# Kernel optimization log

Measured on AMD Instinct MI355X. Metric: run time of the kernel, lower is better.

Reference implementation:

```python
import jax, jax.numpy as jnp
import numpy as np

CH = 32          # channels
HID = CH * 16    # GRU hidden/input size = 512


def setup_inputs() -> dict:
    key = jax.random.key(0)
    ks = jax.random.split(key, 9)
    B, T = 512, 128
    s = 1.0 / np.sqrt(HID)
    frames = jax.random.uniform(ks[0], (B, T, 1, 16, 16), dtype=jnp.float32)
    conv_w = jax.random.normal(ks[1], (CH, 2, 4, 4), jnp.float32) * 0.1
    conv_b = jax.random.normal(ks[2], (CH,), jnp.float32) * 0.01
    w_ih = jax.random.uniform(ks[3], (3 * HID, HID), jnp.float32, -s, s)
    w_hh = jax.random.uniform(ks[4], (3 * HID, HID), jnp.float32, -s, s)
    b_ih = jax.random.uniform(ks[5], (3 * HID,), jnp.float32, -s, s)
    b_hh = jax.random.uniform(ks[6], (3 * HID,), jnp.float32, -s, s)
    deconv_w = jax.random.normal(ks[7], (CH, 1, 4, 4), jnp.float32) * 0.1
    deconv_b = jax.random.normal(ks[8], (1,), jnp.float32) * 0.01
    return {"frames": frames, "conv_w": conv_w, "conv_b": conv_b,
            "w_ih": w_ih, "w_hh": w_hh, "b_ih": b_ih, "b_hh": b_hh,
            "deconv_w": deconv_w, "deconv_b": deconv_b}


def reference(frames, conv_w, conv_b, w_ih, w_hh, b_ih, b_hh, deconv_w, deconv_b):
    B, T = frames.shape[0], frames.shape[1]
    T2 = T - 2
    curr = frames[:, 1:T - 1]              # (B,T2,1,16,16)
    prev = frames[:, :T - 2]               # (B,T2,1,16,16)
    diff = jnp.concatenate([curr, prev], axis=2)  # (B,T2,2,16,16)

    # Encoder: Conv2d(2,CH,4,stride=4). Stride==kernel -> non-overlapping patches.
    # Reshape HxW=16x16 into (i,p,j,q) with H=4i+p, W=4j+q.
    x = diff.reshape(B * T2, 2, 4, 4, 4, 4)                 # (n,c,i,p,j,q)
    enc = jnp.einsum('bcipjq,ocpq->boij', x, conv_w) + conv_b[None, :, None, None]
    feat = jax.nn.gelu(enc, approximate=False).reshape(B, T2, HID)  # flatten(1), exact GELU

    # GRU (single layer, batch_first, zero init hidden)
    gates_x = jnp.einsum('bti,gi->tbg', feat, w_ih) + b_ih  # (T2,B,3H)

    def step(h, gx):
        gh = h @ w_hh.T + b_hh
        gxr, gxz, gxn = jnp.split(gx, 3, axis=-1)
        ghr, ghz, ghn = jnp.split(gh, 3, axis=-1)
        r = jax.nn.sigmoid(gxr + ghr)
        z = jax.nn.sigmoid(gxz + ghz)
        n = jnp.tanh(gxn + r * ghn)
        h_new = (1.0 - z) * n + z * h
        return h_new, h_new

    h0 = jnp.zeros((B, HID), frames.dtype)
    _, outs = jax.lax.scan(step, h0, gates_x)               # (T2,B,HID)

    # Decoder: ConvTranspose2d(CH,1,4,stride=4). Stride==kernel -> scatter patches.
    dec_in = outs.transpose(1, 0, 2).reshape(B * T2, CH, 4, 4)
    dec = jnp.einsum('ncij,copq->noipjq', dec_in, deconv_w).reshape(B * T2, 1, 16, 16)
    delta = jnp.tanh(dec + deconv_b[None, :, None, None])

    pred = jnp.clip(curr.reshape(B * T2, 1, 16, 16) + delta, 0.0, 1.0)
    return pred.reshape(B, T2, 1, 16, 16)
```

## Files before the change

### kernel.cpp

```cpp
#include <hip/hip_runtime.h>
#include <cstdint>

typedef float f32x4 __attribute__((ext_vector_type(4)));
typedef __bf16 bf16x8 __attribute__((ext_vector_type(8)));
typedef unsigned short us8 __attribute__((ext_vector_type(8)));
typedef unsigned int u32x4 __attribute__((ext_vector_type(4)));
typedef unsigned long long u64;

#define T2 126

__device__ __forceinline__ unsigned short f2bf(float x){
  union { float f; uint32_t u; } v; v.f = x;
  return (unsigned short)((v.u + 0x7fffu + ((v.u >> 16) & 1u)) >> 16);
}
__device__ __forceinline__ float bf2f(unsigned short h){
  union { uint32_t u; float f; } v; v.u = ((uint32_t)h) << 16; return v.f;
}
__device__ __forceinline__ f32x4 mfma_bf16(us8 a, us8 b, f32x4 c){
  return __builtin_amdgcn_mfma_f32_16x16x32_bf16(
      __builtin_bit_cast(bf16x8, a), __builtin_bit_cast(bf16x8, b), c, 0, 0, 0);
}
__device__ __forceinline__ float sigm(float x){ return 1.0f / (1.0f + __expf(-x)); }

#define HSWZ(row, chunk) ((row) * 512 + ((((chunk) ^ ((row) & 7))) << 3))

__global__ void __launch_bounds__(256) pack_w_kernel(const float* __restrict__ w,
                                                     unsigned short* __restrict__ dst){
  int tid = blockIdx.x * 256 + threadIdx.x;
  int l = tid & 63;
  int tile = tid >> 6;
  int kt = tile & 15, jt = tile >> 4;
  int row = jt * 16 + (l & 15);
  int col = kt * 32 + (l >> 4) * 8;
  const float* s = w + (size_t)row * 512 + col;
  unsigned short o[8];
  #pragma unroll
  for (int e = 0; e < 8; e++) o[e] = f2bf(s[e]);
  *(us8*)(dst + (size_t)tid * 8) = *(const us8*)o;
}

__global__ void __launch_bounds__(512, 1) gates_gemm_kernel(
    const float* __restrict__ frames,
    const float* __restrict__ cw,
    const float* __restrict__ cb,
    const unsigned short* __restrict__ wih_p,
    const float* __restrict__ b_ih,
    unsigned short* __restrict__ gates_c,
    int t0, int Tc){
  __shared__ unsigned short alds[112 * 512];
  __shared__ float wl[1024];
  __shared__ float cbl[32];
  int tid = threadIdx.x;
  int grp = blockIdx.x & 31;
  int tlc = blockIdx.x >> 5;
  wl[tid] = cw[tid]; wl[tid + 512] = cw[tid + 512];
  if (tid < 32) cbl[tid] = cb[tid];
  __syncthreads();
  #pragma unroll
  for (int tk = 0; tk < 4; tk++){
    int task = tid + 512 * tk;
    if (task < 1792){
      int sA = task >> 4, patch = task & 15;
      int t7 = sA >> 4, i = sA & 15;
      int tl = tlc * 7 + t7;
      int b = grp * 16 + i;
      int t = t0 + tl;
      const float* fb = frames + ((size_t)b * 128 + t) * 256;
      int ii = patch >> 2, jj = patch & 3;
      float4 pv[4], cv[4];
      #pragma unroll
      for (int p = 0; p < 4; p++){
        int base = (ii * 4 + p) * 16 + jj * 4;
        pv[p] = *(const float4*)(fb + base);
        cv[p] = *(const float4*)(fb + 256 + base);
      }
      #pragma unroll
      for (int o = 0; o < 32; o++){
        const float* wc = &wl[o * 32];
        float acc = cbl[o];
        #pragma unroll
        for (int p = 0; p < 4; p++){
          acc += cv[p].x * wc[p*4+0] + cv[p].y * wc[p*4+1]
               + cv[p].z * wc[p*4+2] + cv[p].w * wc[p*4+3];
          acc += pv[p].x * wc[16+p*4+0] + pv[p].y * wc[16+p*4+1]
               + pv[p].z * wc[16+p*4+2] + pv[p].w * wc[16+p*4+3];
        }
        float g = 0.5f * acc * (1.0f + erff(acc * 0.70710678118654752f));
        int col = o * 16 + patch;
        alds[HSWZ(sA, col >> 3) + (col & 7)] = f2bf(g);
      }
    }
  }
  __syncthreads();
  int l = tid & 63, w = tid >> 6;
  int lr = l & 15, lh = l >> 4;
  for (int jg = 0; jg < 3; jg++){
    int jt0 = w * 12 + jg * 4;
    int q4 = w * 3 + jg;
    int g = q4 >> 3, slcT = q4 & 7;
    f32x4 acc[7][4];
    #pragma unroll
    for (int mt = 0; mt < 7; mt++)
      #pragma unroll
      for (int jj = 0; jj < 4; jj++) acc[mt][jj] = (f32x4){0.f,0.f,0.f,0.f};
    #pragma unroll
    for (int kt = 0; kt < 16; kt++){
      us8 a[7], bfr[4];
      #pragma unroll
      for (int mt = 0; mt < 7; mt++)
        a[mt] = *(const us8*)&alds[HSWZ(mt * 16 + lr, kt * 4 + lh)];
      #pragma unroll
      for (int jj = 0; jj < 4; jj++)
        bfr[jj] = *(const us8*)(wih_p + ((size_t)((jt0 + jj) * 16 + kt) * 512 + l * 8));
      #pragma unroll
      for (int mt = 0; mt < 7; mt++)
        #pragma unroll
        for (int jj = 0; jj < 4; jj++)
          acc[mt][jj] = mfma_bf16(a[mt], bfr[jj], acc[mt][jj]);
    }
    #pragma unroll
    for (int jj = 0; jj < 4; jj++){
      float bias = b_ih[(jt0 + jj) * 16 + lr];
      #pragma unroll
      for (int mt = 0; mt < 7; mt++){
        size_t base2 = (((size_t)(tlc * 7 + mt) * 32 + grp) * 8 + slcT) * 3072
                     + g * 1024 + jj * 256 + lr;
        #pragma unroll
        for (int rr = 0; rr < 4; rr++)
          gates_c[base2 + (lh * 4 + rr) * 16] = f2bf(acc[mt][jj][rr] + bias);
      }
    }
  }
}

__global__ void __launch_bounds__(256) scan_init_kernel(u32x4* __restrict__ hq,
                                                        unsigned int* __restrict__ tagbuf){
  int tid = blockIdx.x * 256 + threadIdx.x;
  int stride = gridDim.x * 256;
  for (int i = tid; i < 32768; i += stride)
    hq[i] = (u32x4){0u, 0u, 0u, 0u};
  for (int i = tid; i < 2 * 8 * 32 * 16; i += stride)
    tagbuf[i] = 0u;
}

__global__ void __launch_bounds__(256, 1) gru_scan_kernel(
    const unsigned short* __restrict__ gates_c,
    const unsigned short* __restrict__ whh_p,
    const float* __restrict__ b_hh,
    u32x4* __restrict__ hq,
    unsigned int* __restrict__ tagbuf,
    float* __restrict__ h_state,
    const float* __restrict__ frames,
    const float* __restrict__ dw,
    const float* __restrict__ db,
    float* __restrict__ out,
    int Tc, int t0){
  __shared__ unsigned short hlds[16 * 512];
  __shared__ unsigned short hout[16 * 64];
  __shared__ float dwl[512];
  const int tid = threadIdx.x;
  const int B = blockIdx.x;
  const int grp = B & 31;
  const int slc = B >> 5;
  const int l = tid & 63;
  const int w = tid >> 6;
  const int lr = l & 15, lh = l >> 4;
  const int j = slc * 64 + w * 16 + lr;
  const int rowb = grp * 16;
  const int rloc = lh * 4;

  dwl[tid] = dw[tid]; dwl[tid + 256] = dw[tid + 256];
  const float dbias = db[0];

  us8 wr[16], wz[16], wn[16];
  {
    const int jt = slc * 4 + w;
    #pragma unroll
    for (int kt = 0; kt < 16; kt++){
      wr[kt] = *(volatile const us8*)(whh_p + ((size_t)((jt      ) * 16 + kt) * 512 + l * 8));
      wz[kt] = *(volatile const us8*)(whh_p + ((size_t)((jt + 32) * 16 + kt) * 512 + l * 8));
      wn[kt] = *(volatile const us8*)(whh_p + ((size_t)((jt + 64) * 16 + kt) * 512 + l * 8));
    }
  }
  const float bhr = b_hh[j], bhz = b_hh[512 + j], bhn = b_hh[1024 + j];
  float hprev[4];
  if (t0 == 0){
    hprev[0] = hprev[1] = hprev[2] = hprev[3] = 0.0f;
  } else {
    #pragma unroll
    for (int r = 0; r < 4; r++) hprev[r] = h_state[(size_t)(rowb + rloc + r) * 512 + j];
  }

  auto emit = [&](int so){
    int row = tid >> 4;
    int b = rowb + row;
    const float* fr = frames + ((size_t)b * 128 + so + 1) * 256;
    float* ob = out + ((size_t)b * T2 + so) * 256;
    #pragma unroll
    for (int e = 0; e < 2; e++){
      int pi = (tid & 15) * 2 + e;
      int pr = slc * 2 + (pi >> 4), pc = pi & 15;
      int ii = pr >> 2, pp = pr & 3, jj2 = pc >> 2, qq = pc & 3;
      float acc = dbias;
      #pragma unroll
      for (int c = 0; c < 32; c++){
        int ch = c * 16 + ii * 4 + jj2;
        acc += bf2f(hlds[HSWZ(row, ch >> 3) + (ch & 7)]) * dwl[c * 16 + pp * 4 + qq];
      }
      float dlt = tanhf(acc);
      float rv = fr[pr * 16 + pc] + dlt;
      ob[pr * 16 + pc] = fminf(fmaxf(rv, 0.0f), 1.0f);
    }
  };

  auto poll = [&](int s){
    if (tid < 8){
      const unsigned int* tp = tagbuf + (((size_t)(s & 1) * 8 + tid) * 32 + grp) * 16;
      unsigned int want = (unsigned)s;
      for (;;){
        unsigned int tv;
        asm volatile("global_load_dword %0, %1, off sc0 sc1\n\ts_waitcnt vmcnt(0)"
                     : "=&v"(tv) : "v"(tp) : "memory");
        if (tv >= want) break;
        __builtin_amdgcn_s_sleep(1);
      }
    }
    __syncthreads();
  };

  auto stage = [&](int s){
    const u32x4* rb = hq + (size_t)(s & 1) * 32768;
    int quad = tid & 63, r0 = tid >> 6;
    const u32x4* p0 = rb + ((size_t)(rowb + r0) * 64 + quad);
    const u32x4* p1 = p0 + 4 * 64;
    const u32x4* p2 = p0 + 8 * 64;
    const u32x4* p3 = p0 + 12 * 64;
    u32x4 q0, q1, q2, q3;
    asm volatile(
      "global_load_dwordx4 %0, %4, off sc0 sc1\n\t"
      "global_load_dwordx4 %1, %5, off sc0 sc1\n\t"
      "global_load_dwordx4 %2, %6, off sc0 sc1\n\t"
      "global_load_dwordx4 %3, %7, off sc0 sc1\n\t"
      "s_waitcnt vmcnt(0)"
      : "=&v"(q0), "=&v"(q1), "=&v"(q2), "=&v"(q3)
      : "v"(p0), "v"(p1), "v"(p2), "v"(p3)
      : "memory");
    *(u32x4*)&hlds[HSWZ(r0,      quad)] = q0;
    *(u32x4*)&hlds[HSWZ(r0 + 4,  quad)] = q1;
    *(u32x4*)&hlds[HSWZ(r0 + 8,  quad)] = q2;
    *(u32x4*)&hlds[HSWZ(r0 + 12, quad)] = q3;
    __syncthreads();
  };

  for (int tl = 0; tl < Tc; tl++){
    const int s = t0 + tl;
    const unsigned short* gxp = gates_c
        + ((((size_t)tl * 32 + grp) * 8 + slc) * 3072) + w * 256 + lh * 64 + lr;
    unsigned short gxu[12];
    #pragma unroll
    for (int g = 0; g < 3; g++)
      #pragma unroll
      for (int r = 0; r < 4; r++)
        gxu[g * 4 + r] = gxp[g * 1024 + r * 16];
    poll(s);
    stage(s);
    f32x4 aR = {0.f,0.f,0.f,0.f}, aZ = {0.f,0.f,0.f,0.f}, aN = {0.f,0.f,0.f,0.f};
    #pragma unroll
    for (int kt = 0; kt < 16; kt++){
      us8 a = *(const us8*)&hlds[HSWZ(lr, kt * 4 + lh)];
      aR = mfma_bf16(a, wr[kt], aR);
      aZ = mfma_bf16(a, wz[kt], aZ);
      aN = mfma_bf16(a, wn[kt], aN);
    }
    #pragma unroll
    for (int r = 0; r < 4; r++){
      float rr = sigm(bf2f(gxu[r]) + aR[r] + bhr);
      float zz = sigm(bf2f(gxu[4 + r]) + aZ[r] + bhz);
      float nn = tanhf(bf2f(gxu[8 + r]) + rr * (aN[r] + bhn));
      float hv = (1.0f - zz) * nn + zz * hprev[r];
      hprev[r] = hv;
      hout[(rloc + r) * 64 + w * 16 + lr] = f2bf(hv);
    }
    __syncthreads();
    if (tid < 128){
      int row = tid >> 3, q = tid & 7;
      u32x4 hv = *(const u32x4*)&hout[row * 64 + q * 8];
      u32x4* dst = hq + ((size_t)(((s + 1) & 1) * 512 + rowb + row) * 64 + slc * 8 + q);
      asm volatile("global_store_dwordx4 %0, %1, off sc0 sc1" :: "v"(dst), "v"(hv) : "memory");
    }
    asm volatile("s_waitcnt vmcnt(0)" ::: "memory");
    __syncthreads();
    if (tid == 0){
      unsigned int tg = (unsigned)(s + 1);
      unsigned int* tp = tagbuf + (((size_t)((s + 1) & 1) * 8 + slc) * 32 + grp) * 16;
      asm volatile("global_store_dword %0, %1, off sc0 sc1" :: "v"(tp), "v"(tg) : "memory");
    }
    if (s >= 1) emit(s - 1);
  }
  #pragma unroll
  for (int r = 0; r < 4; r++)
    h_state[(size_t)(rowb + rloc + r) * 512 + j] = hprev[r];
  if (t0 + Tc == T2){
    poll(T2);
    stage(T2);
    emit(T2 - 1);
  }
}

extern "C" void kernel_launch(void* const* d_in, const int* in_sizes, int n_in,
                              void* d_out, int out_size, void* d_ws, size_t ws_size,
                              hipStream_t stream) {
  const float* frames   = (const float*)d_in[0];
  const float* conv_w   = (const float*)d_in[1];
  const float* conv_b   = (const float*)d_in[2];
  const float* w_ih     = (const float*)d_in[3];
  const float* w_hh     = (const float*)d_in[4];
  const float* b_ih     = (const float*)d_in[5];
  const float* b_hh     = (const float*)d_in[6];
  const float* deconv_w = (const float*)d_in[7];
  const float* deconv_b = (const float*)d_in[8];
  float* out = (float*)d_out;
  char* ws = (char*)d_ws;

  unsigned short* wih_p   = (unsigned short*)(ws);
  unsigned short* whh_p   = (unsigned short*)(ws + 1572864LL);
  float*          h_state = (float*)         (ws + 3145728LL);
  u32x4*          hq      = (u32x4*)         (ws + 4194304LL);
  unsigned int*   tagbuf  = (unsigned int*)  (ws + 5242880LL);
  char*           chunkws = ws + 5275648LL;

  static const int divs[6] = {126, 63, 42, 21, 14, 7};
  int Tc = 7;
  for (int i = 0; i < 6; i++){
    long long need = 5275648LL + 1572864LL * divs[i];
    if (need <= (long long)ws_size){ Tc = divs[i]; break; }
  }
  int G = T2 / Tc;

  unsigned short* gates_c = (unsigned short*)(chunkws);

  pack_w_kernel<<<384, 256, 0, stream>>>(w_ih, wih_p);
  pack_w_kernel<<<384, 256, 0, stream>>>(w_hh, whh_p);
  scan_init_kernel<<<64, 256, 0, stream>>>(hq, tagbuf);

  for (int c = 0; c < G; c++){
    int t0 = c * Tc;
    gates_gemm_kernel<<<32 * (Tc / 7), 512, 0, stream>>>(frames, conv_w, conv_b, wih_p,
                                                         b_ih, gates_c, t0, Tc);
    gru_scan_kernel<<<256, 256, 0, stream>>>(gates_c, whh_p, b_hh, hq, tagbuf, h_state,
                                             frames, deconv_w, deconv_b, out,
                                             Tc, t0);
  }
}
```

Measured before the change: 876.9 us.

## Interleave two batch groups per scan block to hide cross-block sync latency

The GRU scan kernel now runs 128 blocks, each handling two 16-row batch groups in alternation. While one group's hidden-state publish and tag store propagate, the block computes the other group. The tag store for a group is deferred until after the next group's staging, which drops the per-step vmcnt wait. The gate layout in the GEMM epilogue is also changed so each lane writes and reads four contiguous bf16 values as a single vector, not four strided scalars. The trade-off is half as many blocks on the GPU, twice the serial work per block, and more LDS and register use.

Measured after the change: 1.767 ms. 2.01x slower.

```diff
diff --git a/kernel.cpp b/kernel.cpp
--- a/kernel.cpp
+++ b/kernel.cpp
@@ -4,8 +4,8 @@
 typedef float f32x4 __attribute__((ext_vector_type(4)));
 typedef __bf16 bf16x8 __attribute__((ext_vector_type(8)));
 typedef unsigned short us8 __attribute__((ext_vector_type(8)));
+typedef unsigned short us4 __attribute__((ext_vector_type(4)));
 typedef unsigned int u32x4 __attribute__((ext_vector_type(4)));
-typedef unsigned long long u64;
 
 #define T2 126
 
@@ -123,11 +123,12 @@
       float bias = b_ih[(jt0 + jj) * 16 + lr];
       #pragma unroll
       for (int mt = 0; mt < 7; mt++){
-        size_t base2 = (((size_t)(tlc * 7 + mt) * 32 + grp) * 8 + slcT) * 3072
-                     + g * 1024 + jj * 256 + lr;
+        unsigned short ov[4];
         #pragma unroll
-        for (int rr = 0; rr < 4; rr++)
-          gates_c[base2 + (lh * 4 + rr) * 16] = f2bf(acc[mt][jj][rr] + bias);
+        for (int rr = 0; rr < 4; rr++) ov[rr] = f2bf(acc[mt][jj][rr] + bias);
+        size_t idx = (((size_t)(tlc * 7 + mt) * 32 + grp) * 8 + slcT) * 3072
+                   + g * 1024 + jj * 256 + lr * 16 + lh * 4;
+        *(us4*)(gates_c + idx) = *(const us4*)ov;
       }
     }
   }
@@ -155,18 +156,21 @@
     const float* __restrict__ db,
     float* __restrict__ out,
     int Tc, int t0){
-  __shared__ unsigned short hlds[16 * 512];
-  __shared__ unsigned short hout[16 * 64];
+  __shared__ unsigned short hldsA[16 * 512];
+  __shared__ unsigned short hldsB[16 * 512];
+  __shared__ unsigned short houtA[16 * 64];
+  __shared__ unsigned short houtB[16 * 64];
   __shared__ float dwl[512];
   const int tid = threadIdx.x;
   const int B = blockIdx.x;
-  const int grp = B & 31;
-  const int slc = B >> 5;
+  const int p = B & 15;
+  const int slc = B >> 4;
+  const int grpA = p * 2, grpB = p * 2 + 1;
+  const int rowbA = p * 32, rowbB = p * 32 + 16;
   const int l = tid & 63;
   const int w = tid >> 6;
   const int lr = l & 15, lh = l >> 4;
   const int j = slc * 64 + w * 16 + lr;
-  const int rowb = grp * 16;
   const int rloc = lh * 4;
 
   dwl[tid] = dw[tid]; dwl[tid + 256] = dw[tid + 256];
@@ -183,42 +187,24 @@
     }
   }
   const float bhr = b_hh[j], bhz = b_hh[512 + j], bhn = b_hh[1024 + j];
-  float hprev[4];
+  float hpA[4], hpB[4];
   if (t0 == 0){
-    hprev[0] = hprev[1] = hprev[2] = hprev[3] = 0.0f;
+    #pragma unroll
+    for (int r = 0; r < 4; r++){ hpA[r] = 0.0f; hpB[r] = 0.0f; }
   } else {
     #pragma unroll
-    for (int r = 0; r < 4; r++) hprev[r] = h_state[(size_t)(rowb + rloc + r) * 512 + j];
-  }
-
-  auto emit = [&](int so){
-    int row = tid >> 4;
-    int b = rowb + row;
-    const float* fr = frames + ((size_t)b * 128 + so + 1) * 256;
-    float* ob = out + ((size_t)b * T2 + so) * 256;
-    #pragma unroll
-    for (int e = 0; e < 2; e++){
-      int pi = (tid & 15) * 2 + e;
-      int pr = slc * 2 + (pi >> 4), pc = pi & 15;
-      int ii = pr >> 2, pp = pr & 3, jj2 = pc >> 2, qq = pc & 3;
-      float acc = dbias;
-      #pragma unroll
-      for (int c = 0; c < 32; c++){
-        int ch = c * 16 + ii * 4 + jj2;
-        acc += bf2f(hlds[HSWZ(row, ch >> 3) + (ch & 7)]) * dwl[c * 16 + pp * 4 + qq];
-      }
-      float dlt = tanhf(acc);
-      float rv = fr[pr * 16 + pc] + dlt;
-      ob[pr * 16 + pc] = fminf(fmaxf(rv, 0.0f), 1.0f);
-    }
-  };
-
-  auto poll = [&](int s){
+    for (int r = 0; r < 4; r++){
+      hpA[r] = h_state[(size_t)(rowbA + rloc + r) * 512 + j];
+      hpB[r] = h_state[(size_t)(rowbB + rloc + r) * 512 + j];
+    }
+  }
+
+  auto poll = [&](int s, int grp){
     if (tid < 8){
       const unsigned int* tp = tagbuf + (((size_t)(s & 1) * 8 + tid) * 32 + grp) * 16;
       unsigned int want = (unsigned)s;
+      unsigned int tv;
       for (;;){
-        unsigned int tv;
         asm volatile("global_load_dword %0, %1, off sc0 sc1\n\ts_waitcnt vmcnt(0)"
                      : "=&v"(tv) : "v"(tp) : "memory");
         if (tv >= want) break;
@@ -228,7 +214,7 @@
     __syncthreads();
   };
 
-  auto stage = [&](int s){
+  auto stage = [&](int s, int rowb, unsigned short* hl){
     const u32x4* rb = hq + (size_t)(s & 1) * 32768;
     int quad = tid & 63, r0 = tid >> 6;
     const u32x4* p0 = rb + ((size_t)(rowb + r0) * 64 + quad);
@@ -245,65 +231,115 @@
       : "=&v"(q0), "=&v"(q1), "=&v"(q2), "=&v"(q3)
       : "v"(p0), "v"(p1), "v"(p2), "v"(p3)
       : "memory");
-    *(u32x4*)&hlds[HSWZ(r0,      quad)] = q0;
-    *(u32x4*)&hlds[HSWZ(r0 + 4,  quad)] = q1;
-    *(u32x4*)&hlds[HSWZ(r0 + 8,  quad)] = q2;
-    *(u32x4*)&hlds[HSWZ(r0 + 12, quad)] = q3;
+    *(u32x4*)&hl[HSWZ(r0,      quad)] = q0;
+    *(u32x4*)&hl[HSWZ(r0 + 4,  quad)] = q1;
+    *(u32x4*)&hl[HSWZ(r0 + 8,  quad)] = q2;
+    *(u32x4*)&hl[HSWZ(r0 + 12, quad)] = q3;
     __syncthreads();
   };
 
-  for (int tl = 0; tl < Tc; tl++){
-    const int s = t0 + tl;
-    const unsigned short* gxp = gates_c
-        + ((((size_t)tl * 32 + grp) * 8 + slc) * 3072) + w * 256 + lh * 64 + lr;
-    unsigned short gxu[12];
-    #pragma unroll
-    for (int g = 0; g < 3; g++)
-      #pragma unroll
-      for (int r = 0; r < 4; r++)
-        gxu[g * 4 + r] = gxp[g * 1024 + r * 16];
-    poll(s);
-    stage(s);
+  auto tagstore = [&](int sval, int grp){
+    if (tid == 0){
+      unsigned int tg = (unsigned)sval;
+      unsigned int* tp = tagbuf + (((size_t)(sval & 1) * 8 + slc) * 32 + grp) * 16;
+      asm volatile("global_store_dword %0, %1, off sc0 sc1" :: "v"(tp), "v"(tg) : "memory");
+    }
+  };
+
+  auto gru = [&](const unsigned short* hl, us4 gR, us4 gZ, us4 gN,
+                 float* hp, unsigned short* ho){
     f32x4 aR = {0.f,0.f,0.f,0.f}, aZ = {0.f,0.f,0.f,0.f}, aN = {0.f,0.f,0.f,0.f};
     #pragma unroll
     for (int kt = 0; kt < 16; kt++){
-      us8 a = *(const us8*)&hlds[HSWZ(lr, kt * 4 + lh)];
+      us8 a = *(const us8*)&hl[HSWZ(lr, kt * 4 + lh)];
       aR = mfma_bf16(a, wr[kt], aR);
       aZ = mfma_bf16(a, wz[kt], aZ);
       aN = mfma_bf16(a, wn[kt], aN);
     }
     #pragma unroll
     for (int r = 0; r < 4; r++){
-      float rr = sigm(bf2f(gxu[r]) + aR[r] + bhr);
-      float zz = sigm(bf2f(gxu[4 + r]) + aZ[r] + bhz);
-      float nn = tanhf(bf2f(gxu[8 + r]) + rr * (aN[r] + bhn));
-      float hv = (1.0f - zz) * nn + zz * hprev[r];
-      hprev[r] = hv;
-      hout[(rloc + r) * 64 + w * 16 + lr] = f2bf(hv);
-    }
-    __syncthreads();
+      float rr = sigm(bf2f(gR[r]) + aR[r] + bhr);
+      float zz = sigm(bf2f(gZ[r]) + aZ[r] + bhz);
+      float nn = tanhf(bf2f(gN[r]) + rr * (aN[r] + bhn));
+      float hv = (1.0f - zz) * nn + zz * hp[r];
+      hp[r] = hv;
+      ho[(rloc + r) * 64 + w * 16 + lr] = f2bf(hv);
+    }
+  };
+
+  auto publish = [&](int s, int rowb, const unsigned short* ho){
     if (tid < 128){
       int row = tid >> 3, q = tid & 7;
-      u32x4 hv = *(const u32x4*)&hout[row * 64 + q * 8];
+      u32x4 hv = *(const u32x4*)&ho[row * 64 + q * 8];
       u32x4* dst = hq + ((size_t)(((s + 1) & 1) * 512 + rowb + row) * 64 + slc * 8 + q);
       asm volatile("global_store_dwordx4 %0, %1, off sc0 sc1" :: "v"(dst), "v"(hv) : "memory");
     }
-    asm volatile("s_waitcnt vmcnt(0)" ::: "memory");
+  };
+
+  auto emit = [&](int so, int rowb, const unsigned short* hl){
+    int row = tid >> 4;
+    int b = rowb + row;
+    const float* fr = frames + ((size_t)b * 128 + so + 1) * 256;
+    float* ob = out + ((size_t)b * T2 + so) * 256;
+    #pragma unroll
+    for (int e = 0; e < 2; e++){
+      int pi = (tid & 15) * 2 + e;
+      int pr = slc * 2 + (pi >> 4), pc = pi & 15;
+      int ii = pr >> 2, pp = pr & 3, jj2 = pc >> 2, qq = pc & 3;
+      float acc = dbias;
+      #pragma unroll
+      for (int c = 0; c < 32; c++){
+        int ch = c * 16 + ii * 4 + jj2;
+        acc += bf2f(hl[HSWZ(row, ch >> 3) + (ch & 7)]) * dwl[c * 16 + pp * 4 + qq];
+      }
+      float dlt = tanhf(acc);
+      float rv = fr[pr * 16 + pc] + dlt;
+      ob[pr * 16 + pc] = fminf(fmaxf(rv, 0.0f), 1.0f);
+    }
+  };
+
+  for (int tl = 0; tl < Tc; tl++){
+    const int s = t0 + tl;
+    const unsigned short* gxpA = gates_c
+        + ((((size_t)tl * 32 + grpA) * 8 + slc) * 3072) + w * 256 + lr * 16 + lh * 4;
+    us4 gRA = *(const us4*)(gxpA);
+    us4 gZA = *(const us4*)(gxpA + 1024);
+    us4 gNA = *(const us4*)(gxpA + 2048);
+    poll(s, grpA);
+    stage(s, rowbA, hldsA);
+    if (tl > 0) tagstore(s, grpB);
+    gru(hldsA, gRA, gZA, gNA, hpA, houtA);
     __syncthreads();
-    if (tid == 0){
-      unsigned int tg = (unsigned)(s + 1);
-      unsigned int* tp = tagbuf + (((size_t)((s + 1) & 1) * 8 + slc) * 32 + grp) * 16;
-      asm volatile("global_store_dword %0, %1, off sc0 sc1" :: "v"(tp), "v"(tg) : "memory");
-    }
-    if (s >= 1) emit(s - 1);
-  }
+    publish(s, rowbA, houtA);
+    if (s >= 1) emit(s - 1, rowbA, hldsA);
+    const unsigned short* gxpB = gates_c
+        + ((((size_t)tl * 32 + grpB) * 8 + slc) * 3072) + w * 256 + lr * 16 + lh * 4;
+    us4 gRB = *(const us4*)(gxpB);
+    us4 gZB = *(const us4*)(gxpB + 1024);
+    us4 gNB = *(const us4*)(gxpB + 2048);
+    poll(s, grpB);
+    stage(s, rowbB, hldsB);
+    tagstore(s + 1, grpA);
+    gru(hldsB, gRB, gZB, gNB, hpB, houtB);
+    __syncthreads();
+    publish(s, rowbB, houtB);
+    if (s >= 1) emit(s - 1, rowbB, hldsB);
+  }
+  asm volatile("s_waitcnt vmcnt(0)" ::: "memory");
+  __syncthreads();
+  tagstore(t0 + Tc, grpB);
   #pragma unroll
-  for (int r = 0; r < 4; r++)
-    h_state[(size_t)(rowb + rloc + r) * 512 + j] = hprev[r];
+  for (int r = 0; r < 4; r++){
+    h_state[(size_t)(rowbA + rloc + r) * 512 + j] = hpA[r];
+    h_state[(size_t)(rowbB + rloc + r) * 512 + j] = hpB[r];
+  }
   if (t0 + Tc == T2){
-    poll(T2);
-    stage(T2);
-    emit(T2 - 1);
+    poll(T2, grpA);
+    stage(T2, rowbA, hldsA);
+    emit(T2 - 1, rowbA, hldsA);
+    poll(T2, grpB);
+    stage(T2, rowbB, hldsB);
+    emit(T2 - 1, rowbB, hldsB);
   }
 }
 
@@ -347,8 +383,8 @@
     int t0 = c * Tc;
     gates_gemm_kernel<<<32 * (Tc / 7), 512, 0, stream>>>(frames, conv_w, conv_b, wih_p,
                                                          b_ih, gates_c, t0, Tc);
-    gru_scan_kernel<<<256, 256, 0, stream>>>(gates_c, whh_p, b_hh, hq, tagbuf, h_state,
-                                             frames, deconv_w, deconv_b, out,
+    gru_scan_kernel<<<128, 256, 0, stream>>>(gates_c, whh_p, b_hh, hq, tagbuf,
+                                             h_state, frames, deconv_w, deconv_b, out,
                                              Tc, t0);
   }
 }
```

## Fuse conv+GELU and input-gate GEMM into the persistent GRU scan kernel

Applied to the files above, without the earlier changes.

Removes the separate gates GEMM kernel and the chunked gate buffer in global memory. Each scan block now computes conv+GELU features for its 16 batch rows and the input-gate projection for its own 64-column slice one step ahead, double-buffered in LDS. This drops the launches per chunk, the global writes and reads of the gate buffer, and the h_state save and restore. In exchange the serial loop gains extra per-step work (conv, 48 MFMAs with W_ih streamed from global or L2 each step) and extra barriers. Only partly overlapped with the cross-block polling.

New measurement: 1.912 ms. 118% more time.

```diff
diff --git a/kernel.cpp b/kernel.cpp
--- a/kernel.cpp
+++ b/kernel.cpp
@@ -5,7 +5,6 @@
 typedef __bf16 bf16x8 __attribute__((ext_vector_type(8)));
 typedef unsigned short us8 __attribute__((ext_vector_type(8)));
 typedef unsigned int u32x4 __attribute__((ext_vector_type(4)));
-typedef unsigned long long u64;
 
 #define T2 126
 
@@ -39,100 +38,6 @@
   *(us8*)(dst + (size_t)tid * 8) = *(const us8*)o;
 }
 
-__global__ void __launch_bounds__(512, 1) gates_gemm_kernel(
-    const float* __restrict__ frames,
-    const float* __restrict__ cw,
-    const float* __restrict__ cb,
-    const unsigned short* __restrict__ wih_p,
-    const float* __restrict__ b_ih,
-    unsigned short* __restrict__ gates_c,
-    int t0, int Tc){
-  __shared__ unsigned short alds[112 * 512];
-  __shared__ float wl[1024];
-  __shared__ float cbl[32];
-  int tid = threadIdx.x;
-  int grp = blockIdx.x & 31;
-  int tlc = blockIdx.x >> 5;
-  wl[tid] = cw[tid]; wl[tid + 512] = cw[tid + 512];
-  if (tid < 32) cbl[tid] = cb[tid];
-  __syncthreads();
-  #pragma unroll
-  for (int tk = 0; tk < 4; tk++){
-    int task = tid + 512 * tk;
-    if (task < 1792){
-      int sA = task >> 4, patch = task & 15;
-      int t7 = sA >> 4, i = sA & 15;
-      int tl = tlc * 7 + t7;
-      int b = grp * 16 + i;
-      int t = t0 + tl;
-      const float* fb = frames + ((size_t)b * 128 + t) * 256;
-      int ii = patch >> 2, jj = patch & 3;
-      float4 pv[4], cv[4];
-      #pragma unroll
-      for (int p = 0; p < 4; p++){
-        int base = (ii * 4 + p) * 16 + jj * 4;
-        pv[p] = *(const float4*)(fb + base);
-        cv[p] = *(const float4*)(fb + 256 + base);
-      }
-      #pragma unroll
-      for (int o = 0; o < 32; o++){
-        const float* wc = &wl[o * 32];
-        float acc = cbl[o];
-        #pragma unroll
-        for (int p = 0; p < 4; p++){
-          acc += cv[p].x * wc[p*4+0] + cv[p].y * wc[p*4+1]
-               + cv[p].z * wc[p*4+2] + cv[p].w * wc[p*4+3];
-          acc += pv[p].x * wc[16+p*4+0] + pv[p].y * wc[16+p*4+1]
-               + pv[p].z * wc[16+p*4+2] + pv[p].w * wc[16+p*4+3];
-        }
-        float g = 0.5f * acc * (1.0f + erff(acc * 0.70710678118654752f));
-        int col = o * 16 + patch;
-        alds[HSWZ(sA, col >> 3) + (col & 7)] = f2bf(g);
-      }
-    }
-  }
-  __syncthreads();
-  int l = tid & 63, w = tid >> 6;
-  int lr = l & 15, lh = l >> 4;
-  for (int jg = 0; jg < 3; jg++){
-    int jt0 = w * 12 + jg * 4;
-    int q4 = w * 3 + jg;
-    int g = q4 >> 3, slcT = q4 & 7;
-    f32x4 acc[7][4];
-    #pragma unroll
-    for (int mt = 0; mt < 7; mt++)
-      #pragma unroll
-      for (int jj = 0; jj < 4; jj++) acc[mt][jj] = (f32x4){0.f,0.f,0.f,0.f};
-    #pragma unroll
-    for (int kt = 0; kt < 16; kt++){
-      us8 a[7], bfr[4];
-      #pragma unroll
-      for (int mt = 0; mt < 7; mt++)
-        a[mt] = *(const us8*)&alds[HSWZ(mt * 16 + lr, kt * 4 + lh)];
-      #pragma unroll
-      for (int jj = 0; jj < 4; jj++)
-        bfr[jj] = *(const us8*)(wih_p + ((size_t)((jt0 + jj) * 16 + kt) * 512 + l * 8));
-      #pragma unroll
-      for (int mt = 0; mt < 7; mt++)
-        #pragma unroll
-        for (int jj = 0; jj < 4; jj++)
-          acc[mt][jj] = mfma_bf16(a[mt], bfr[jj], acc[mt][jj]);
-    }
-    #pragma unroll
-    for (int jj = 0; jj < 4; jj++){
-      float bias = b_ih[(jt0 + jj) * 16 + lr];
-      #pragma unroll
-      for (int mt = 0; mt < 7; mt++){
-        size_t base2 = (((size_t)(tlc * 7 + mt) * 32 + grp) * 8 + slcT) * 3072
-                     + g * 1024 + jj * 256 + lr;
-        #pragma unroll
-        for (int rr = 0; rr < 4; rr++)
-          gates_c[base2 + (lh * 4 + rr) * 16] = f2bf(acc[mt][jj][rr] + bias);
-      }
-    }
-  }
-}
-
 __global__ void __launch_bounds__(256) scan_init_kernel(u32x4* __restrict__ hq,
                                                         unsigned int* __restrict__ tagbuf){
   int tid = blockIdx.x * 256 + threadIdx.x;
@@ -144,20 +49,25 @@
 }
 
 __global__ void __launch_bounds__(256, 1) gru_scan_kernel(
-    const unsigned short* __restrict__ gates_c,
     const unsigned short* __restrict__ whh_p,
+    const unsigned short* __restrict__ wih_p,
     const float* __restrict__ b_hh,
+    const float* __restrict__ b_ih,
     u32x4* __restrict__ hq,
     unsigned int* __restrict__ tagbuf,
-    float* __restrict__ h_state,
     const float* __restrict__ frames,
+    const float* __restrict__ cw,
+    const float* __restrict__ cb,
     const float* __restrict__ dw,
     const float* __restrict__ db,
-    float* __restrict__ out,
-    int Tc, int t0){
+    float* __restrict__ out){
   __shared__ unsigned short hlds[16 * 512];
+  __shared__ unsigned short featl[16 * 512];
+  __shared__ unsigned short gbuf[2][3 * 16 * 72];
   __shared__ unsigned short hout[16 * 64];
+  __shared__ float wl[1024];
   __shared__ float dwl[512];
+  __shared__ float cbl[32];
   const int tid = threadIdx.x;
   const int B = blockIdx.x;
   const int grp = B & 31;
@@ -170,6 +80,9 @@
   const int rloc = lh * 4;
 
   dwl[tid] = dw[tid]; dwl[tid + 256] = dw[tid + 256];
+  wl[tid] = cw[tid]; wl[tid + 256] = cw[tid + 256];
+  wl[tid + 512] = cw[tid + 512]; wl[tid + 768] = cw[tid + 768];
+  if (tid < 32) cbl[tid] = cb[tid];
   const float dbias = db[0];
 
   us8 wr[16], wz[16], wn[16];
@@ -183,33 +96,63 @@
     }
   }
   const float bhr = b_hh[j], bhz = b_hh[512 + j], bhn = b_hh[1024 + j];
-  float hprev[4];
-  if (t0 == 0){
-    hprev[0] = hprev[1] = hprev[2] = hprev[3] = 0.0f;
-  } else {
-    #pragma unroll
-    for (int r = 0; r < 4; r++) hprev[r] = h_state[(size_t)(rowb + rloc + r) * 512 + j];
+
+  int jtg[3], gg[3], wtt[3]; float gbias[3];
+  #pragma unroll
+  for (int jj = 0; jj < 3; jj++){
+    int q = w * 3 + jj; gg[jj] = q >> 2; wtt[jj] = q & 3;
+    jtg[jj] = gg[jj] * 32 + slc * 4 + wtt[jj];
+    gbias[jj] = b_ih[gg[jj] * 512 + slc * 64 + wtt[jj] * 16 + lr];
   }
-
-  auto emit = [&](int so){
-    int row = tid >> 4;
-    int b = rowb + row;
-    const float* fr = frames + ((size_t)b * 128 + so + 1) * 256;
-    float* ob = out + ((size_t)b * T2 + so) * 256;
-    #pragma unroll
-    for (int e = 0; e < 2; e++){
-      int pi = (tid & 15) * 2 + e;
-      int pr = slc * 2 + (pi >> 4), pc = pi & 15;
-      int ii = pr >> 2, pp = pr & 3, jj2 = pc >> 2, qq = pc & 3;
-      float acc = dbias;
+  float hprev[4] = {0.0f, 0.0f, 0.0f, 0.0f};
+  __syncthreads();
+
+  auto convgelu = [&](int u){
+    int i = tid >> 4, patch = tid & 15;
+    const float* fb = frames + ((size_t)(rowb + i) * 128 + u) * 256;
+    int ii = patch >> 2, jjp = patch & 3;
+    float4 pv[4], cv[4];
+    #pragma unroll
+    for (int p = 0; p < 4; p++){
+      int base = (ii * 4 + p) * 16 + jjp * 4;
+      pv[p] = *(const float4*)(fb + base);
+      cv[p] = *(const float4*)(fb + 256 + base);
+    }
+    #pragma unroll
+    for (int o = 0; o < 32; o++){
+      const float* wc = &wl[o * 32];
+      float acc = cbl[o];
       #pragma unroll
-      for (int c = 0; c < 32; c++){
-        int ch = c * 16 + ii * 4 + jj2;
-        acc += bf2f(hlds[HSWZ(row, ch >> 3) + (ch & 7)]) * dwl[c * 16 + pp * 4 + qq];
+      for (int p = 0; p < 4; p++){
+        acc += cv[p].x * wc[p*4+0] + cv[p].y * wc[p*4+1]
+             + cv[p].z * wc[p*4+2] + cv[p].w * wc[p*4+3];
+        acc += pv[p].x * wc[16+p*4+0] + pv[p].y * wc[16+p*4+1]
+             + pv[p].z * wc[16+p*4+2] + pv[p].w * wc[16+p*4+3];
       }
-      float dlt = tanhf(acc);
-      float rv = fr[pr * 16 + pc] + dlt;
-      ob[pr * 16 + pc] = fminf(fmaxf(rv, 0.0f), 1.0f);
+      float g = 0.5f * acc * (1.0f + erff(acc * 0.70710678118654752f));
+      int col = o * 16 + patch;
+      featl[HSWZ(i, col >> 3) + (col & 7)] = f2bf(g);
+    }
+  };
+
+  auto gatesgemm = [&](int par){
+    f32x4 a0 = {0.f,0.f,0.f,0.f}, a1 = {0.f,0.f,0.f,0.f}, a2 = {0.f,0.f,0.f,0.f};
+    #pragma unroll
+    for (int kt = 0; kt < 16; kt++){
+      us8 a = *(const us8*)&featl[HSWZ(lr, kt * 4 + lh)];
+      us8 b0 = *(const us8*)(wih_p + ((size_t)(jtg[0] * 16 + kt) * 512 + l * 8));
+      us8 b1 = *(const us8*)(wih_p + ((size_t)(jtg[1] * 16 + kt) * 512 + l * 8));
+      us8 b2 = *(const us8*)(wih_p + ((size_t)(jtg[2] * 16 + kt) * 512 + l * 8));
+      a0 = mfma_bf16(a, b0, a0);
+      a1 = mfma_bf16(a, b1, a1);
+      a2 = mfma_bf16(a, b2, a2);
+    }
+    unsigned short* gb = &gbuf[par][0];
+    #pragma unroll
+    for (int r = 0; r < 4; r++){
+      gb[(gg[0] * 16 + lh * 4 + r) * 72 + wtt[0] * 16 + lr] = f2bf(a0[r] + gbias[0]);
+      gb[(gg[1] * 16 + lh * 4 + r) * 72 + wtt[1] * 16 + lr] = f2bf(a1[r] + gbias[1]);
+      gb[(gg[2] * 16 + lh * 4 + r) * 72 + wtt[2] * 16 + lr] = f2bf(a2[r] + gbias[2]);
     }
   };
 
@@ -217,8 +160,8 @@
     if (tid < 8){
       const unsigned int* tp = tagbuf + (((size_t)(s & 1) * 8 + tid) * 32 + grp) * 16;
       unsigned int want = (unsigned)s;
+      unsigned int tv;
       for (;;){
-        unsigned int tv;
         asm volatile("global_load_dword %0, %1, off sc0 sc1\n\ts_waitcnt vmcnt(0)"
                      : "=&v"(tv) : "v"(tp) : "memory");
         if (tv >= want) break;
@@ -252,16 +195,39 @@
     __syncthreads();
   };
 
-  for (int tl = 0; tl < Tc; tl++){
-    const int s = t0 + tl;
-    const unsigned short* gxp = gates_c
-        + ((((size_t)tl * 32 + grp) * 8 + slc) * 3072) + w * 256 + lh * 64 + lr;
-    unsigned short gxu[12];
-    #pragma unroll
-    for (int g = 0; g < 3; g++)
+  auto emit = [&](int so){
+    int row = tid >> 4;
+    int b = rowb + row;
+    const float* fr = frames + ((size_t)b * 128 + so + 1) * 256;
+    float* ob = out + ((size_t)b * T2 + so) * 256;
+    #pragma unroll
+    for (int e = 0; e < 2; e++){
+      int pi = (tid & 15) * 2 + e;
+      int pr = slc * 2 + (pi >> 4), pc = pi & 15;
+      int ii = pr >> 2, pp = pr & 3, jj2 = pc >> 2, qq = pc & 3;
+      float acc = dbias;
       #pragma unroll
-      for (int r = 0; r < 4; r++)
-        gxu[g * 4 + r] = gxp[g * 1024 + r * 16];
+      for (int c = 0; c < 32; c++){
+        int ch = c * 16 + ii * 4 + jj2;
+        acc += bf2f(hlds[HSWZ(row, ch >> 3) + (ch & 7)]) * dwl[c * 16 + pp * 4 + qq];
+      }
+      float dlt = tanhf(acc);
+      float rv = fr[pr * 16 + pc] + dlt;
+      ob[pr * 16 + pc] = fminf(fmaxf(rv, 0.0f), 1.0f);
+    }
+  };
+
+  convgelu(0);
+  __syncthreads();
+  gatesgemm(0);
+
+  for (int s = 0; s < T2; s++){
+    if (s + 1 < T2){
+      __syncthreads();
+      convgelu(s + 1);
+      __syncthreads();
+      gatesgemm((s + 1) & 1);
+    }
     poll(s);
     stage(s);
     f32x4 aR = {0.f,0.f,0.f,0.f}, aZ = {0.f,0.f,0.f,0.f}, aN = {0.f,0.f,0.f,0.f};
@@ -272,11 +238,15 @@
       aZ = mfma_bf16(a, wz[kt], aZ);
       aN = mfma_bf16(a, wn[kt], aN);
     }
+    const unsigned short* gb = &gbuf[s & 1][0];
     #pragma unroll
     for (int r = 0; r < 4; r++){
-      float rr = sigm(bf2f(gxu[r]) + aR[r] + bhr);
-      float zz = sigm(bf2f(gxu[4 + r]) + aZ[r] + bhz);
-      float nn = tanhf(bf2f(gxu[8 + r]) + rr * (aN[r] + bhn));
+      float gxr = bf2f(gb[(      rloc + r) * 72 + w * 16 + lr]);
+      float gxz = bf2f(gb[(16 + rloc + r) * 72 + w * 16 + lr]);
+      float gxn = bf2f(gb[(32 + rloc + r) * 72 + w * 16 + lr]);
+      float rr = sigm(gxr + aR[r] + bhr);
+      float zz = sigm(gxz + aZ[r] + bhz);
+      float nn = tanhf(gxn + rr * (aN[r] + bhn));
       float hv = (1.0f - zz) * nn + zz * hprev[r];
       hprev[r] = hv;
       hout[(rloc + r) * 64 + w * 16 + lr] = f2bf(hv);
@@ -297,14 +267,9 @@
     }
     if (s >= 1) emit(s - 1);
   }
-  #pragma unroll
-  for (int r = 0; r < 4; r++)
-    h_state[(size_t)(rowb + rloc + r) * 512 + j] = hprev[r];
-  if (t0 + Tc == T2){
-    poll(T2);
-    stage(T2);
-    emit(T2 - 1);
-  }
+  poll(T2);
+  stage(T2);
+  emit(T2 - 1);
 }
 
 extern "C" void kernel_launch(void* const* d_in, const int* in_sizes, int n_in,
@@ -322,33 +287,15 @@
   float* out = (float*)d_out;
   char* ws = (char*)d_ws;
 
-  unsigned short* wih_p   = (unsigned short*)(ws);
-  unsigned short* whh_p   = (unsigned short*)(ws + 1572864LL);
-  float*          h_state = (float*)         (ws + 3145728LL);
-  u32x4*          hq      = (u32x4*)         (ws + 4194304LL);
-  unsigned int*   tagbuf  = (unsigned int*)  (ws + 5242880LL);
-  char*           chunkws = ws + 5275648LL;
-
-  static const int divs[6] = {126, 63, 42, 21, 14, 7};
-  int Tc = 7;
-  for (int i = 0; i < 6; i++){
-    long long need = 5275648LL + 1572864LL * divs[i];
-    if (need <= (long long)ws_size){ Tc = divs[i]; break; }
-  }
-  int G = T2 / Tc;
-
-  unsigned short* gates_c = (unsigned short*)(chunkws);
+  unsigned short* wih_p  = (unsigned short*)(ws);
+  unsigned short* whh_p  = (unsigned short*)(ws + 1572864LL);
+  u32x4*          hq     = (u32x4*)         (ws + 3145728LL);
+  unsigned int*   tagbuf = (unsigned int*)  (ws + 4194304LL);
 
   pack_w_kernel<<<384, 256, 0, stream>>>(w_ih, wih_p);
   pack_w_kernel<<<384, 256, 0, stream>>>(w_hh, whh_p);
   scan_init_kernel<<<64, 256, 0, stream>>>(hq, tagbuf);
-
-  for (int c = 0; c < G; c++){
-    int t0 = c * Tc;
-    gates_gemm_kernel<<<32 * (Tc / 7), 512, 0, stream>>>(frames, conv_w, conv_b, wih_p,
-                                                         b_ih, gates_c, t0, Tc);
-    gru_scan_kernel<<<256, 256, 0, stream>>>(gates_c, whh_p, b_hh, hq, tagbuf, h_state,
-                                             frames, deconv_w, deconv_b, out,
-                                             Tc, t0);
-  }
-}
+  gru_scan_kernel<<<256, 256, 0, stream>>>(whh_p, wih_p, b_hh, b_ih, hq, tagbuf,
+                                           frames, conv_w, conv_b,
+                                           deconv_w, deconv_b, out);
+}
```
